# Kernel tuning notes

Hardware: AMD Instinct MI355X
Metric: run time of the kernel (lower is better)

The kernel has to match this reference:

```python
import jax, jax.numpy as jnp
import numpy as np

LN_EPS = 1e-5

def _layernorm(x, g, b):
    m = jnp.mean(x, axis=-1, keepdims=True)
    v = jnp.mean((x - m) ** 2, axis=-1, keepdims=True)
    return (x - m) / jnp.sqrt(v + LN_EPS) * g + b

def _mlp(x, w1, g1, b1, w2, g2, b2):
    # Linear(no bias) -> LayerNorm -> Linear(no bias) -> LayerNorm -> ReLU
    x = _layernorm(x @ w1, g1, b1)
    x = _layernorm(x @ w2, g2, b2)
    return jax.nn.relu(x)

def setup_inputs() -> dict:
    key = jax.random.key(0)
    ks = jax.random.split(key, 16)
    Lc, Lf, N, Dc, Df, K = 1024, 4096, 32, 256, 128, 8
    inv = lambda d: 1.0 / np.sqrt(d)
    inp = {
        "features_coarse": jax.random.normal(ks[0], (Lc, N, Dc), dtype=jnp.float32),
        "features_fine": jax.random.normal(ks[1], (Lf, N, Df), dtype=jnp.float32),
        # mlp_coarse: d_in=Dc, d_ff=Df, d_out=Df
        "w1c": jax.random.uniform(ks[2], (Dc, Df), jnp.float32, -inv(Dc), inv(Dc)),
        "g1c": jnp.ones((Df,), jnp.float32),
        "b1c": jnp.zeros((Df,), jnp.float32),
        "w2c": jax.random.uniform(ks[3], (Df, Df), jnp.float32, -inv(Df), inv(Df)),
        "g2c": jnp.ones((Df,), jnp.float32),
        "b2c": jnp.zeros((Df,), jnp.float32),
        # mlp_fine: d_in=Df, d_ff=Df, d_out=Df
        "w1f": jax.random.uniform(ks[4], (Df, Df), jnp.float32, -inv(Df), inv(Df)),
        "g1f": jnp.ones((Df,), jnp.float32),
        "b1f": jnp.zeros((Df,), jnp.float32),
        "w2f": jax.random.uniform(ks[5], (Df, Df), jnp.float32, -inv(Df), inv(Df)),
        "g2f": jnp.ones((Df,), jnp.float32),
        "b2f": jnp.zeros((Df,), jnp.float32),
        "neighbor_row": jax.random.randint(ks[6], (K * Lc * N,), 0, Lf, dtype=jnp.int64 if jax.config.jax_enable_x64 else jnp.int32),
        "neighbor_col": jax.random.randint(ks[7], (K * Lc * N,), 0, N, dtype=jnp.int64 if jax.config.jax_enable_x64 else jnp.int32),
        "keep_idx": jax.random.randint(ks[8], (Lc,), 0, Lf, dtype=jnp.int64 if jax.config.jax_enable_x64 else jnp.int32),
    }
    return inp

def reference(features_coarse, features_fine, w1c, g1c, b1c, w2c, g2c, b2c,
              w1f, g1f, b1f, w2f, g2f, b2f, neighbor_row, neighbor_col, keep_idx):
    Lc, N, Dc = features_coarse.shape
    Lf, _, Df = features_fine.shape
    D = Df
    fc = _mlp(features_coarse, w1c, g1c, b1c, w2c, g2c, b2c)  # (Lc, N, D)
    ff = _mlp(features_fine, w1f, g1f, b1f, w2f, g2f, b2f)    # (Lf, N, D)
    gathered = ff[neighbor_row, neighbor_col]                  # (K*Lc*N, D)
    updated = fc[None] + gathered.reshape(-1, Lc, N, D)        # (K, Lc, N, D)
    ff = ff.at[neighbor_row, neighbor_col].set(updated.reshape(-1, D))
    return ff
```

## Files before the change

### kernel.cpp

```cpp
#include <hip/hip_runtime.h>
#include <hip/hip_bf16.h>

typedef __attribute__((ext_vector_type(8))) short s8v;
typedef __attribute__((ext_vector_type(4))) float f4v;

__device__ __forceinline__ short f2bf(float f) {
    __hip_bfloat16 h = __float2bfloat16(f);
    union { __hip_bfloat16 h; short s; } u{h};
    return u.s;
}
__device__ __forceinline__ float bf2f(unsigned short v) {
    union { unsigned u; float f; } x; x.u = ((unsigned)v) << 16; return x.f;
}

__global__ void pack_kernel(const float* __restrict__ w1c, const float* __restrict__ w2c,
                            const float* __restrict__ w1f, const float* __restrict__ w2f,
                            short* __restrict__ p1c, short* __restrict__ p2c,
                            short* __restrict__ p1f, short* __restrict__ p2f)
{
    int id = blockIdx.x * 256 + threadIdx.x;
    int f  = id >> 6, l = id & 63;
    const float* W; short* P; int fl;
    if      (f < 64)  { W = w1c; P = p1c; fl = f; }
    else if (f < 96)  { W = w2c; P = p2c; fl = f - 64; }
    else if (f < 128) { W = w1f; P = p1f; fl = f - 96; }
    else              { W = w2f; P = p2f; fl = f - 128; }
    int g = l >> 4, c = l & 15;
    int ks = fl >> 3, n = fl & 7;
    s8v o;
    #pragma unroll
    for (int e = 0; e < 8; ++e)
        o[e] = f2bf(W[(ks*32 + g*8 + e) * 128 + n*16 + c]);
    *(s8v*)(P + ((fl*64 + l) << 3)) = o;
}

template<int K1, bool FINE>
__global__ __launch_bounds__(256, 4)
void mlp_mfma(const float* __restrict__ X,
              const short* __restrict__ Wp1,
              const float* __restrict__ g1v, const float* __restrict__ b1v,
              const short* __restrict__ Wp2,
              const float* __restrict__ g2v, const float* __restrict__ b2v,
              float* __restrict__ outF,
              unsigned short* __restrict__ outB,
              const int* __restrict__ winner,
              const unsigned short* __restrict__ fcB,
              const int* __restrict__ nr, const int* __restrict__ nc,
              int* __restrict__ win, int nWinBlocks)
{
    __shared__ short H[4][16][128];

    if (blockIdx.x < (unsigned)nWinBlocks) {
        int i = blockIdx.x * 256 + threadIdx.x;
        atomicMax(&win[nr[i] * 32 + nc[i]], i);
        return;
    }
    const int bid = blockIdx.x - nWinBlocks;

    const int t = threadIdx.x;
    const int wave = t >> 6, lane = t & 63;
    const int g = lane >> 4, c = lane & 15;
    const int wrow = bid * 64 + wave * 16;

    int wv = 0;
    if constexpr (FINE) wv = winner[wrow + c];

    float G1[8], B1[8];
    #pragma unroll
    for (int n = 0; n < 8; ++n) { G1[n] = g1v[n*16 + c]; B1[n] = b1v[n*16 + c]; }

    f4v acc[8];
    #pragma unroll
    for (int n = 0; n < 8; ++n) acc[n] = (f4v){0.f, 0.f, 0.f, 0.f};

    const float* pa = X + (size_t)(wrow + c) * K1 + g*8;
    const short* wp1 = Wp1 + (lane << 3);
    float4 a0 = *(const float4*)pa;
    float4 a1 = *(const float4*)(pa + 4);
    #pragma unroll
    for (int ks = 0; ks < K1/32; ++ks) {
        s8v bfr[8];
        #pragma unroll
        for (int n = 0; n < 8; ++n)
            bfr[n] = *(const s8v*)(wp1 + ((ks*8 + n) << 9));
        s8v af;
        af[0] = f2bf(a0.x); af[1] = f2bf(a0.y); af[2] = f2bf(a0.z); af[3] = f2bf(a0.w);
        af[4] = f2bf(a1.x); af[5] = f2bf(a1.y); af[6] = f2bf(a1.z); af[7] = f2bf(a1.w);
        if (ks + 1 < K1/32) {
            a0 = *(const float4*)(pa + (ks+1)*32);
            a1 = *(const float4*)(pa + (ks+1)*32 + 4);
        }
        #pragma unroll
        for (int n = 0; n < 8; ++n)
            acc[n] = __builtin_amdgcn_mfma_f32_16x16x32_bf16(af, bfr[n], acc[n], 0, 0, 0);
    }

    #pragma unroll
    for (int j = 0; j < 4; ++j) {
        float sm = 0.f, sq = 0.f;
        #pragma unroll
        for (int n = 0; n < 8; ++n) { float v = acc[n][j]; sm += v; sq += v*v; }
        #pragma unroll
        for (int m = 1; m < 16; m <<= 1) {
            sm += __shfl_xor(sm, m, 64);
            sq += __shfl_xor(sq, m, 64);
        }
        float mean = sm * (1.f/128.f);
        float rstd = rsqrtf(sq * (1.f/128.f) - mean*mean + 1e-5f);
        int row = g*4 + j;
        #pragma unroll
        for (int n = 0; n < 8; ++n) {
            float y = (acc[n][j] - mean) * rstd * G1[n] + B1[n];
            int col = n*16 + c;
            int phys = (((col >> 3) ^ row) << 3) | (col & 7);
            H[wave][row][phys] = f2bf(y);
        }
    }

    f4v acc2[8];
    #pragma unroll
    for (int n = 0; n < 8; ++n) acc2[n] = (f4v){0.f, 0.f, 0.f, 0.f};

    const short* wp2 = Wp2 + (lane << 3);
    #pragma unroll
    for (int ks = 0; ks < 4; ++ks) {
        s8v bfr[8];
        #pragma unroll
        for (int n = 0; n < 8; ++n)
            bfr[n] = *(const s8v*)(wp2 + ((ks*8 + n) << 9));
        s8v af = *(const s8v*)&H[wave][c][((ks*4 + g) ^ c) << 3];
        #pragma unroll
        for (int n = 0; n < 8; ++n)
            acc2[n] = __builtin_amdgcn_mfma_f32_16x16x32_bf16(af, bfr[n], acc2[n], 0, 0, 0);
    }

    float G2[8], B2[8];
    #pragma unroll
    for (int n = 0; n < 8; ++n) { G2[n] = g2v[n*16 + c]; B2[n] = b2v[n*16 + c]; }
    #pragma unroll
    for (int j = 0; j < 4; ++j) {
        float sm = 0.f, sq = 0.f;
        #pragma unroll
        for (int n = 0; n < 8; ++n) { float v = acc2[n][j]; sm += v; sq += v*v; }
        #pragma unroll
        for (int m = 1; m < 16; m <<= 1) {
            sm += __shfl_xor(sm, m, 64);
            sq += __shfl_xor(sq, m, 64);
        }
        float mean = sm * (1.f/128.f);
        float rstd = rsqrtf(sq * (1.f/128.f) - mean*mean + 1e-5f);
        int R = wrow + g*4 + j;
        float y[8];
        #pragma unroll
        for (int n = 0; n < 8; ++n)
            y[n] = fmaxf((acc2[n][j] - mean) * rstd * G2[n] + B2[n], 0.f);
        if constexpr (FINE) {
            int w = __shfl(wv, g*4 + j, 64);
            if (w >= 0) {
                const unsigned short* fp = fcB + (size_t)(w & 32767) * 128 + c;
                #pragma unroll
                for (int n = 0; n < 8; ++n) y[n] += bf2f(fp[n*16]);
            }
            float* op = outF + (size_t)R * 128 + c;
            #pragma unroll
            for (int n = 0; n < 8; ++n) op[n*16] = y[n];
        } else {
            unsigned short* op = outB + (size_t)R * 128 + c;
            #pragma unroll
            for (int n = 0; n < 8; ++n) op[n*16] = (unsigned short)f2bf(y[n]);
        }
    }
}

extern "C" void kernel_launch(void* const* d_in, const int* in_sizes, int n_in,
                              void* d_out, int out_size, void* d_ws, size_t ws_size,
                              hipStream_t stream)
{
    const float* fcoarse = (const float*)d_in[0];
    const float* ffine   = (const float*)d_in[1];
    const float* w1c = (const float*)d_in[2];
    const float* g1c = (const float*)d_in[3];
    const float* b1c = (const float*)d_in[4];
    const float* w2c = (const float*)d_in[5];
    const float* g2c = (const float*)d_in[6];
    const float* b2c = (const float*)d_in[7];
    const float* w1f = (const float*)d_in[8];
    const float* g1f = (const float*)d_in[9];
    const float* b1f = (const float*)d_in[10];
    const float* w2f = (const float*)d_in[11];
    const float* g2f = (const float*)d_in[12];
    const float* b2f = (const float*)d_in[13];
    const int* nrow  = (const int*)d_in[14];
    const int* ncol  = (const int*)d_in[15];

    float* out = (float*)d_out;

    const int Mc = 32768, Mf = 131072;

    unsigned short* fcB = (unsigned short*)d_ws;
    char* base = (char*)d_ws;
    int*   winner = (int*)(base + 8u*1024*1024);
    short* p1c = (short*)(base + 8u*1024*1024 + 512u*1024);
    short* p2c = p1c + 256*128;
    short* p1f = p2c + 128*128;
    short* p2f = p1f + 128*128;

    hipMemsetAsync(winner, 0xFF, (size_t)Mf * sizeof(int), stream);
    pack_kernel<<<40, 256, 0, stream>>>(w1c, w2c, w1f, w2f, p1c, p2c, p1f, p2f);

    mlp_mfma<256, false><<<1024 + Mc/64, 256, 0, stream>>>(
        fcoarse, p1c, g1c, b1c, p2c, g2c, b2c,
        nullptr, fcB, nullptr, nullptr,
        nrow, ncol, winner, 1024);

    mlp_mfma<128, true><<<Mf/64, 256, 0, stream>>>(
        ffine, p1f, g1f, b1f, p2f, g2f, b2f,
        out, nullptr, winner, fcB,
        nullptr, nullptr, nullptr, 0);
}
```

Baseline: 81.04 us.

## Process 64 rows per wave to reuse weight fragments and vectorize output stores

```diff
diff --git a/kernel.cpp b/kernel.cpp
--- a/kernel.cpp
+++ b/kernel.cpp
@@ -35,7 +35,7 @@
 }
 
 template<int K1, bool FINE>
-__global__ __launch_bounds__(256, 4)
+__global__ __launch_bounds__(256, 2)
 void mlp_mfma(const float* __restrict__ X,
               const short* __restrict__ Wp1,
               const float* __restrict__ g1v, const float* __restrict__ b1v,
@@ -48,7 +48,7 @@
               const int* __restrict__ nr, const int* __restrict__ nc,
               int* __restrict__ win, int nWinBlocks)
 {
-    __shared__ short H[4][16][128];
+    __shared__ short H[4][64][128];
 
     if (blockIdx.x < (unsigned)nWinBlocks) {
         int i = blockIdx.x * 256 + threadIdx.x;
@@ -60,66 +60,76 @@
     const int t = threadIdx.x;
     const int wave = t >> 6, lane = t & 63;
     const int g = lane >> 4, c = lane & 15;
-    const int wrow = bid * 64 + wave * 16;
+    const int wrow = bid * 256 + wave * 64;
 
     int wv = 0;
-    if constexpr (FINE) wv = winner[wrow + c];
+    if constexpr (FINE) wv = winner[wrow + lane];
 
     float G1[8], B1[8];
     #pragma unroll
     for (int n = 0; n < 8; ++n) { G1[n] = g1v[n*16 + c]; B1[n] = b1v[n*16 + c]; }
 
-    f4v acc[8];
-    #pragma unroll
-    for (int n = 0; n < 8; ++n) acc[n] = (f4v){0.f, 0.f, 0.f, 0.f};
-
-    const float* pa = X + (size_t)(wrow + c) * K1 + g*8;
+    f4v acc[4][8];
+    #pragma unroll
+    for (int s = 0; s < 4; ++s)
+        #pragma unroll
+        for (int n = 0; n < 8; ++n) acc[s][n] = (f4v){0.f, 0.f, 0.f, 0.f};
+
     const short* wp1 = Wp1 + (lane << 3);
-    float4 a0 = *(const float4*)pa;
-    float4 a1 = *(const float4*)(pa + 4);
     #pragma unroll
     for (int ks = 0; ks < K1/32; ++ks) {
         s8v bfr[8];
         #pragma unroll
         for (int n = 0; n < 8; ++n)
             bfr[n] = *(const s8v*)(wp1 + ((ks*8 + n) << 9));
-        s8v af;
-        af[0] = f2bf(a0.x); af[1] = f2bf(a0.y); af[2] = f2bf(a0.z); af[3] = f2bf(a0.w);
-        af[4] = f2bf(a1.x); af[5] = f2bf(a1.y); af[6] = f2bf(a1.z); af[7] = f2bf(a1.w);
-        if (ks + 1 < K1/32) {
-            a0 = *(const float4*)(pa + (ks+1)*32);
-            a1 = *(const float4*)(pa + (ks+1)*32 + 4);
-        }
-        #pragma unroll
-        for (int n = 0; n < 8; ++n)
-            acc[n] = __builtin_amdgcn_mfma_f32_16x16x32_bf16(af, bfr[n], acc[n], 0, 0, 0);
-    }
-
-    #pragma unroll
-    for (int j = 0; j < 4; ++j) {
-        float sm = 0.f, sq = 0.f;
-        #pragma unroll
-        for (int n = 0; n < 8; ++n) { float v = acc[n][j]; sm += v; sq += v*v; }
-        #pragma unroll
-        for (int m = 1; m < 16; m <<= 1) {
-            sm += __shfl_xor(sm, m, 64);
-            sq += __shfl_xor(sq, m, 64);
-        }
-        float mean = sm * (1.f/128.f);
-        float rstd = rsqrtf(sq * (1.f/128.f) - mean*mean + 1e-5f);
-        int row = g*4 + j;
-        #pragma unroll
-        for (int n = 0; n < 8; ++n) {
-            float y = (acc[n][j] - mean) * rstd * G1[n] + B1[n];
-            int col = n*16 + c;
-            int phys = (((col >> 3) ^ row) << 3) | (col & 7);
-            H[wave][row][phys] = f2bf(y);
-        }
-    }
-
-    f4v acc2[8];
-    #pragma unroll
-    for (int n = 0; n < 8; ++n) acc2[n] = (f4v){0.f, 0.f, 0.f, 0.f};
+        s8v af[4];
+        #pragma unroll
+        for (int s = 0; s < 4; ++s) {
+            const float* p = X + (size_t)(wrow + s*16 + c) * K1 + ks*32 + g*8;
+            float4 a0 = *(const float4*)p;
+            float4 a1 = *(const float4*)(p + 4);
+            s8v v;
+            v[0] = f2bf(a0.x); v[1] = f2bf(a0.y); v[2] = f2bf(a0.z); v[3] = f2bf(a0.w);
+            v[4] = f2bf(a1.x); v[5] = f2bf(a1.y); v[6] = f2bf(a1.z); v[7] = f2bf(a1.w);
+            af[s] = v;
+        }
+        #pragma unroll
+        for (int s = 0; s < 4; ++s)
+            #pragma unroll
+            for (int n = 0; n < 8; ++n)
+                acc[s][n] = __builtin_amdgcn_mfma_f32_16x16x32_bf16(af[s], bfr[n], acc[s][n], 0, 0, 0);
+    }
+
+    #pragma unroll
+    for (int s = 0; s < 4; ++s) {
+        #pragma unroll
+        for (int j = 0; j < 4; ++j) {
+            float sm = 0.f, sq = 0.f;
+            #pragma unroll
+            for (int n = 0; n < 8; ++n) { float v = acc[s][n][j]; sm += v; sq += v*v; }
+            #pragma unroll
+            for (int m = 1; m < 16; m <<= 1) {
+                sm += __shfl_xor(sm, m, 64);
+                sq += __shfl_xor(sq, m, 64);
+            }
+            float mean = sm * (1.f/128.f);
+            float rstd = rsqrtf(sq * (1.f/128.f) - mean*mean + 1e-5f);
+            int row = s*16 + g*4 + j;
+            #pragma unroll
+            for (int n = 0; n < 8; ++n) {
+                float y = (acc[s][n][j] - mean) * rstd * G1[n] + B1[n];
+                int col = n*16 + c;
+                int phys = (((col >> 3) ^ (row & 15)) << 3) | (col & 7);
+                H[wave][row][phys] = f2bf(y);
+            }
+        }
+    }
+
+    f4v acc2[4][8];
+    #pragma unroll
+    for (int s = 0; s < 4; ++s)
+        #pragma unroll
+        for (int n = 0; n < 8; ++n) acc2[s][n] = (f4v){0.f, 0.f, 0.f, 0.f};
 
     const short* wp2 = Wp2 + (lane << 3);
     #pragma unroll
@@ -128,46 +138,67 @@
         #pragma unroll
         for (int n = 0; n < 8; ++n)
             bfr[n] = *(const s8v*)(wp2 + ((ks*8 + n) << 9));
-        s8v af = *(const s8v*)&H[wave][c][((ks*4 + g) ^ c) << 3];
-        #pragma unroll
-        for (int n = 0; n < 8; ++n)
-            acc2[n] = __builtin_amdgcn_mfma_f32_16x16x32_bf16(af, bfr[n], acc2[n], 0, 0, 0);
+        s8v af[4];
+        #pragma unroll
+        for (int s = 0; s < 4; ++s)
+            af[s] = *(const s8v*)&H[wave][s*16 + c][((ks*4 + g) ^ c) << 3];
+        #pragma unroll
+        for (int s = 0; s < 4; ++s)
+            #pragma unroll
+            for (int n = 0; n < 8; ++n)
+                acc2[s][n] = __builtin_amdgcn_mfma_f32_16x16x32_bf16(af[s], bfr[n], acc2[s][n], 0, 0, 0);
     }
 
     float G2[8], B2[8];
     #pragma unroll
     for (int n = 0; n < 8; ++n) { G2[n] = g2v[n*16 + c]; B2[n] = b2v[n*16 + c]; }
     #pragma unroll
-    for (int j = 0; j < 4; ++j) {
-        float sm = 0.f, sq = 0.f;
-        #pragma unroll
-        for (int n = 0; n < 8; ++n) { float v = acc2[n][j]; sm += v; sq += v*v; }
-        #pragma unroll
-        for (int m = 1; m < 16; m <<= 1) {
-            sm += __shfl_xor(sm, m, 64);
-            sq += __shfl_xor(sq, m, 64);
-        }
-        float mean = sm * (1.f/128.f);
-        float rstd = rsqrtf(sq * (1.f/128.f) - mean*mean + 1e-5f);
-        int R = wrow + g*4 + j;
-        float y[8];
-        #pragma unroll
-        for (int n = 0; n < 8; ++n)
-            y[n] = fmaxf((acc2[n][j] - mean) * rstd * G2[n] + B2[n], 0.f);
+    for (int s = 0; s < 4; ++s) {
+        #pragma unroll
+        for (int j = 0; j < 4; ++j) {
+            float sm = 0.f, sq = 0.f;
+            #pragma unroll
+            for (int n = 0; n < 8; ++n) { float v = acc2[s][n][j]; sm += v; sq += v*v; }
+            #pragma unroll
+            for (int m = 1; m < 16; m <<= 1) {
+                sm += __shfl_xor(sm, m, 64);
+                sq += __shfl_xor(sq, m, 64);
+            }
+            float mean = sm * (1.f/128.f);
+            float rstd = rsqrtf(sq * (1.f/128.f) - mean*mean + 1e-5f);
+            int row = s*16 + g*4 + j;
+            #pragma unroll
+            for (int n = 0; n < 8; ++n) {
+                float y = fmaxf((acc2[s][n][j] - mean) * rstd * G2[n] + B2[n], 0.f);
+                int col = n*16 + c;
+                int phys = (((col >> 3) ^ (row & 15)) << 3) | (col & 7);
+                H[wave][row][phys] = f2bf(y);
+            }
+        }
+    }
+
+    #pragma unroll
+    for (int it = 0; it < 16; ++it) {
+        int row = it*4 + g;
+        int R   = wrow + row;
+        s8v v = *(const s8v*)&H[wave][row][(c ^ (row & 15)) << 3];
         if constexpr (FINE) {
-            int w = __shfl(wv, g*4 + j, 64);
+            float y8[8];
+            #pragma unroll
+            for (int e = 0; e < 8; ++e) y8[e] = bf2f((unsigned short)v[e]);
+            int w = __shfl(wv, row, 64);
             if (w >= 0) {
-                const unsigned short* fp = fcB + (size_t)(w & 32767) * 128 + c;
+                const s8v u = *(const s8v*)(fcB + (size_t)(w & 32767) * 128 + c*8);
                 #pragma unroll
-                for (int n = 0; n < 8; ++n) y[n] += bf2f(fp[n*16]);
-            }
-            float* op = outF + (size_t)R * 128 + c;
-            #pragma unroll
-            for (int n = 0; n < 8; ++n) op[n*16] = y[n];
+                for (int e = 0; e < 8; ++e) y8[e] += bf2f((unsigned short)u[e]);
+            }
+            float4 o0 = {y8[0], y8[1], y8[2], y8[3]};
+            float4 o1 = {y8[4], y8[5], y8[6], y8[7]};
+            float* op = outF + (size_t)R * 128 + c*8;
+            *(float4*)op       = o0;
+            *(float4*)(op + 4) = o1;
         } else {
-            unsigned short* op = outB + (size_t)R * 128 + c;
-            #pragma unroll
-            for (int n = 0; n < 8; ++n) op[n*16] = (unsigned short)f2bf(y[n]);
+            *(s8v*)(outB + (size_t)R * 128 + c*8) = v;
         }
     }
 }
@@ -208,12 +239,12 @@
     hipMemsetAsync(winner, 0xFF, (size_t)Mf * sizeof(int), stream);
     pack_kernel<<<40, 256, 0, stream>>>(w1c, w2c, w1f, w2f, p1c, p2c, p1f, p2f);
 
-    mlp_mfma<256, false><<<1024 + Mc/64, 256, 0, stream>>>(
+    mlp_mfma<256, false><<<1024 + Mc/256, 256, 0, stream>>>(
         fcoarse, p1c, g1c, b1c, p2c, g2c, b2c,
         nullptr, fcB, nullptr, nullptr,
         nrow, ncol, winner, 1024);
 
-    mlp_mfma<128, true><<<Mf/64, 256, 0, stream>>>(
+    mlp_mfma<128, true><<<Mf/256, 256, 0, stream>>>(
         ffine, p1f, g1f, b1f, p2f, g2f, b2f,
         out, nullptr, winner, fcB,
         nullptr, nullptr, nullptr, 0);
```

New measurement: 121.9 us. +50.5%, slower.

## Fold first LayerNorm into second GEMM weights and pass activations via shuffles

Applied to the files above, without the earlier changes.

```diff
diff --git a/kernel.cpp b/kernel.cpp
--- a/kernel.cpp
+++ b/kernel.cpp
@@ -12,34 +12,62 @@
 __device__ __forceinline__ float bf2f(unsigned short v) {
     union { unsigned u; float f; } x; x.u = ((unsigned)v) << 16; return x.f;
 }
-
-__global__ void pack_kernel(const float* __restrict__ w1c, const float* __restrict__ w2c,
+__device__ __forceinline__ unsigned packbf(float a, float b) {
+    return (unsigned)(unsigned short)f2bf(a) | ((unsigned)(unsigned short)f2bf(b) << 16);
+}
+
+__global__ void prep_kernel(const float* __restrict__ w1c, const float* __restrict__ w2c,
+                            const float* __restrict__ g1c, const float* __restrict__ b1c,
                             const float* __restrict__ w1f, const float* __restrict__ w2f,
+                            const float* __restrict__ g1f, const float* __restrict__ b1f,
                             short* __restrict__ p1c, short* __restrict__ p2c,
-                            short* __restrict__ p1f, short* __restrict__ p2f)
+                            short* __restrict__ p1f, short* __restrict__ p2f,
+                            float* __restrict__ s2c, float* __restrict__ bwc,
+                            float* __restrict__ s2f, float* __restrict__ bwf)
 {
-    int id = blockIdx.x * 256 + threadIdx.x;
+    int b = blockIdx.x, t = threadIdx.x;
+    if (b >= 40) {
+        if (t >= 128) return;
+        const float* W  = (b == 40) ? w2c : w2f;
+        const float* g1 = (b == 40) ? g1c : g1f;
+        const float* b1 = (b == 40) ? b1c : b1f;
+        float* s2 = (b == 40) ? s2c : s2f;
+        float* bw = (b == 40) ? bwc : bwf;
+        float s = 0.f, w2sum = 0.f;
+        for (int k = 0; k < 128; ++k) {
+            float wv = W[k * 128 + t];
+            s     += bf2f((unsigned short)f2bf(g1[k] * wv));
+            w2sum += b1[k] * wv;
+        }
+        s2[t] = s; bw[t] = w2sum;
+        return;
+    }
+    int id = b * 256 + t;
     int f  = id >> 6, l = id & 63;
-    const float* W; short* P; int fl;
+    const float* W; const float* g1 = nullptr; short* P; int fl;
     if      (f < 64)  { W = w1c; P = p1c; fl = f; }
-    else if (f < 96)  { W = w2c; P = p2c; fl = f - 64; }
+    else if (f < 96)  { W = w2c; P = p2c; fl = f - 64;  g1 = g1c; }
     else if (f < 128) { W = w1f; P = p1f; fl = f - 96; }
-    else              { W = w2f; P = p2f; fl = f - 128; }
+    else              { W = w2f; P = p2f; fl = f - 128; g1 = g1f; }
     int g = l >> 4, c = l & 15;
     int ks = fl >> 3, n = fl & 7;
     s8v o;
     #pragma unroll
-    for (int e = 0; e < 8; ++e)
-        o[e] = f2bf(W[(ks*32 + g*8 + e) * 128 + n*16 + c]);
+    for (int e = 0; e < 8; ++e) {
+        int k = ks*32 + g*8 + e;
+        float v = W[k * 128 + n*16 + c];
+        if (g1) v *= g1[k];
+        o[e] = f2bf(v);
+    }
     *(s8v*)(P + ((fl*64 + l) << 3)) = o;
 }
 
 template<int K1, bool FINE>
 __global__ __launch_bounds__(256, 4)
 void mlp_mfma(const float* __restrict__ X,
-              const short* __restrict__ Wp1,
-              const float* __restrict__ g1v, const float* __restrict__ b1v,
-              const short* __restrict__ Wp2,
+              const short* __restrict__ WpA,
+              const short* __restrict__ WpB,
+              const float* __restrict__ s2v, const float* __restrict__ bwv,
               const float* __restrict__ g2v, const float* __restrict__ b2v,
               float* __restrict__ outF,
               unsigned short* __restrict__ outB,
@@ -48,126 +76,156 @@
               const int* __restrict__ nr, const int* __restrict__ nc,
               int* __restrict__ win, int nWinBlocks)
 {
-    __shared__ short H[4][16][128];
-
     if (blockIdx.x < (unsigned)nWinBlocks) {
         int i = blockIdx.x * 256 + threadIdx.x;
         atomicMax(&win[nr[i] * 32 + nc[i]], i);
         return;
     }
-    const int bid = blockIdx.x - nWinBlocks;
-
-    const int t = threadIdx.x;
+    const int bid  = blockIdx.x - nWinBlocks;
+    const int t    = threadIdx.x;
     const int wave = t >> 6, lane = t & 63;
-    const int g = lane >> 4, c = lane & 15;
-    const int wrow = bid * 64 + wave * 16;
+    const int G = lane >> 4, n16 = lane & 15;
+    const int row = bid * 64 + wave * 16 + n16;
+    const size_t rowK = (size_t)row * K1;
 
     int wv = 0;
-    if constexpr (FINE) wv = winner[wrow + c];
-
-    float G1[8], B1[8];
-    #pragma unroll
-    for (int n = 0; n < 8; ++n) { G1[n] = g1v[n*16 + c]; B1[n] = b1v[n*16 + c]; }
-
-    f4v acc[8];
-    #pragma unroll
-    for (int n = 0; n < 8; ++n) acc[n] = (f4v){0.f, 0.f, 0.f, 0.f};
-
-    const float* pa = X + (size_t)(wrow + c) * K1 + g*8;
-    const short* wp1 = Wp1 + (lane << 3);
-    float4 a0 = *(const float4*)pa;
-    float4 a1 = *(const float4*)(pa + 4);
-    #pragma unroll
-    for (int ks = 0; ks < K1/32; ++ks) {
-        s8v bfr[8];
-        #pragma unroll
-        for (int n = 0; n < 8; ++n)
-            bfr[n] = *(const s8v*)(wp1 + ((ks*8 + n) << 9));
-        s8v af;
-        af[0] = f2bf(a0.x); af[1] = f2bf(a0.y); af[2] = f2bf(a0.z); af[3] = f2bf(a0.w);
-        af[4] = f2bf(a1.x); af[5] = f2bf(a1.y); af[6] = f2bf(a1.z); af[7] = f2bf(a1.w);
-        if (ks + 1 < K1/32) {
-            a0 = *(const float4*)(pa + (ks+1)*32);
-            a1 = *(const float4*)(pa + (ks+1)*32 + 4);
-        }
-        #pragma unroll
-        for (int n = 0; n < 8; ++n)
-            acc[n] = __builtin_amdgcn_mfma_f32_16x16x32_bf16(af, bfr[n], acc[n], 0, 0, 0);
-    }
-
-    #pragma unroll
-    for (int j = 0; j < 4; ++j) {
-        float sm = 0.f, sq = 0.f;
-        #pragma unroll
-        for (int n = 0; n < 8; ++n) { float v = acc[n][j]; sm += v; sq += v*v; }
-        #pragma unroll
-        for (int m = 1; m < 16; m <<= 1) {
-            sm += __shfl_xor(sm, m, 64);
-            sq += __shfl_xor(sq, m, 64);
-        }
-        float mean = sm * (1.f/128.f);
-        float rstd = rsqrtf(sq * (1.f/128.f) - mean*mean + 1e-5f);
-        int row = g*4 + j;
-        #pragma unroll
-        for (int n = 0; n < 8; ++n) {
-            float y = (acc[n][j] - mean) * rstd * G1[n] + B1[n];
-            int col = n*16 + c;
-            int phys = (((col >> 3) ^ row) << 3) | (col & 7);
-            H[wave][row][phys] = f2bf(y);
-        }
+    if constexpr (FINE) wv = winner[row];
+
+    f4v acc1[8];
+    #pragma unroll
+    for (int mt = 0; mt < 8; ++mt) acc1[mt] = (f4v){0.f, 0.f, 0.f, 0.f};
+
+    const short* wpa = WpA + (lane << 3);
+    const float* pX  = X + rowK + G*8;
+    #pragma unroll
+    for (int kb = 0; kb < K1/32; kb += 4) {
+        float4 aPf[4][2];
+        #pragma unroll
+        for (int k2 = 0; k2 < 4; ++k2) {
+            aPf[k2][0] = *(const float4*)(pX + (kb + k2)*32);
+            aPf[k2][1] = *(const float4*)(pX + (kb + k2)*32 + 4);
+        }
+        #pragma unroll
+        for (int k2 = 0; k2 < 4; ++k2) {
+            const int ks = kb + k2;
+            s8v wfr[8];
+            #pragma unroll
+            for (int mt = 0; mt < 8; ++mt)
+                wfr[mt] = *(const s8v*)(wpa + ((ks*8 + mt) << 9));
+            s8v xf;
+            xf[0] = f2bf(aPf[k2][0].x); xf[1] = f2bf(aPf[k2][0].y);
+            xf[2] = f2bf(aPf[k2][0].z); xf[3] = f2bf(aPf[k2][0].w);
+            xf[4] = f2bf(aPf[k2][1].x); xf[5] = f2bf(aPf[k2][1].y);
+            xf[6] = f2bf(aPf[k2][1].z); xf[7] = f2bf(aPf[k2][1].w);
+            #pragma unroll
+            for (int mt = 0; mt < 8; ++mt)
+                acc1[mt] = __builtin_amdgcn_mfma_f32_16x16x32_bf16(wfr[mt], xf, acc1[mt], 0, 0, 0);
+        }
+    }
+
+    float sm = 0.f, sq = 0.f;
+    #pragma unroll
+    for (int mt = 0; mt < 8; ++mt)
+        #pragma unroll
+        for (int j = 0; j < 4; ++j) { float v = acc1[mt][j]; sm += v; sq += v*v; }
+    sm += __shfl_xor(sm, 16, 64); sm += __shfl_xor(sm, 32, 64);
+    sq += __shfl_xor(sq, 16, 64); sq += __shfl_xor(sq, 32, 64);
+    const float mean1 = sm * (1.f/128.f);
+    const float rstd1 = rsqrtf(sq * (1.f/128.f) - mean1*mean1 + 1e-5f);
+
+    unsigned pk[8][2];
+    #pragma unroll
+    for (int mt = 0; mt < 8; ++mt) {
+        pk[mt][0] = packbf(acc1[mt][0], acc1[mt][1]);
+        pk[mt][1] = packbf(acc1[mt][2], acc1[mt][3]);
     }
 
     f4v acc2[8];
     #pragma unroll
-    for (int n = 0; n < 8; ++n) acc2[n] = (f4v){0.f, 0.f, 0.f, 0.f};
-
-    const short* wp2 = Wp2 + (lane << 3);
+    for (int mt = 0; mt < 8; ++mt) acc2[mt] = (f4v){0.f, 0.f, 0.f, 0.f};
+
+    const short* wpb = WpB + (lane << 3);
+    const int src0 = ((G & 1) << 5) + n16;
+    const int src1 = src0 + 16;
+    const bool hiG = (G >= 2);
     #pragma unroll
     for (int ks = 0; ks < 4; ++ks) {
-        s8v bfr[8];
-        #pragma unroll
-        for (int n = 0; n < 8; ++n)
-            bfr[n] = *(const s8v*)(wp2 + ((ks*8 + n) << 9));
-        s8v af = *(const s8v*)&H[wave][c][((ks*4 + g) ^ c) << 3];
-        #pragma unroll
-        for (int n = 0; n < 8; ++n)
-            acc2[n] = __builtin_amdgcn_mfma_f32_16x16x32_bf16(af, bfr[n], acc2[n], 0, 0, 0);
-    }
-
-    float G2[8], B2[8];
-    #pragma unroll
-    for (int n = 0; n < 8; ++n) { G2[n] = g2v[n*16 + c]; B2[n] = b2v[n*16 + c]; }
-    #pragma unroll
-    for (int j = 0; j < 4; ++j) {
-        float sm = 0.f, sq = 0.f;
-        #pragma unroll
-        for (int n = 0; n < 8; ++n) { float v = acc2[n][j]; sm += v; sq += v*v; }
-        #pragma unroll
-        for (int m = 1; m < 16; m <<= 1) {
-            sm += __shfl_xor(sm, m, 64);
-            sq += __shfl_xor(sq, m, 64);
-        }
-        float mean = sm * (1.f/128.f);
-        float rstd = rsqrtf(sq * (1.f/128.f) - mean*mean + 1e-5f);
-        int R = wrow + g*4 + j;
-        float y[8];
-        #pragma unroll
-        for (int n = 0; n < 8; ++n)
-            y[n] = fmaxf((acc2[n][j] - mean) * rstd * G2[n] + B2[n], 0.f);
-        if constexpr (FINE) {
-            int w = __shfl(wv, g*4 + j, 64);
-            if (w >= 0) {
-                const unsigned short* fp = fcB + (size_t)(w & 32767) * 128 + c;
-                #pragma unroll
-                for (int n = 0; n < 8; ++n) y[n] += bf2f(fp[n*16]);
+        int r00 = __shfl((int)pk[2*ks][0],   src0, 64);
+        int r01 = __shfl((int)pk[2*ks][1],   src0, 64);
+        int r02 = __shfl((int)pk[2*ks][0],   src1, 64);
+        int r03 = __shfl((int)pk[2*ks][1],   src1, 64);
+        int r10 = __shfl((int)pk[2*ks+1][0], src0, 64);
+        int r11 = __shfl((int)pk[2*ks+1][1], src0, 64);
+        int r12 = __shfl((int)pk[2*ks+1][0], src1, 64);
+        int r13 = __shfl((int)pk[2*ks+1][1], src1, 64);
+        union { int u[4]; s8v v; } hb;
+        hb.u[0] = hiG ? r10 : r00; hb.u[1] = hiG ? r11 : r01;
+        hb.u[2] = hiG ? r12 : r02; hb.u[3] = hiG ? r13 : r03;
+        s8v wfr[8];
+        #pragma unroll
+        for (int mt = 0; mt < 8; ++mt)
+            wfr[mt] = *(const s8v*)(wpb + ((ks*8 + mt) << 9));
+        #pragma unroll
+        for (int mt = 0; mt < 8; ++mt)
+            acc2[mt] = __builtin_amdgcn_mfma_f32_16x16x32_bf16(wfr[mt], hb.v, acc2[mt], 0, 0, 0);
+    }
+
+    float h2[8][4];
+    float sm2 = 0.f, sq2 = 0.f;
+    #pragma unroll
+    for (int mt = 0; mt < 8; ++mt) {
+        const int col = mt*16 + G*4;
+        f4v s2l = *(const f4v*)&s2v[col];
+        f4v bwl = *(const f4v*)&bwv[col];
+        #pragma unroll
+        for (int j = 0; j < 4; ++j) {
+            float v = rstd1 * (acc2[mt][j] - mean1 * s2l[j]) + bwl[j];
+            h2[mt][j] = v; sm2 += v; sq2 += v*v;
+        }
+    }
+    sm2 += __shfl_xor(sm2, 16, 64); sm2 += __shfl_xor(sm2, 32, 64);
+    sq2 += __shfl_xor(sq2, 16, 64); sq2 += __shfl_xor(sq2, 32, 64);
+    const float mean2 = sm2 * (1.f/128.f);
+    const float rstd2 = rsqrtf(sq2 * (1.f/128.f) - mean2*mean2 + 1e-5f);
+
+    if constexpr (FINE) {
+        ushort4 gv[8];
+        const bool hasw = (wv >= 0);
+        const size_t src = (size_t)(wv & 32767) * 128;
+        if (hasw) {
+            #pragma unroll
+            for (int mt = 0; mt < 8; ++mt)
+                gv[mt] = *(const ushort4*)(fcB + src + mt*16 + G*4);
+        }
+        #pragma unroll
+        for (int mt = 0; mt < 8; ++mt) {
+            const int col = mt*16 + G*4;
+            f4v g2l = *(const f4v*)&g2v[col];
+            f4v b2l = *(const f4v*)&b2v[col];
+            float4 o;
+            float z0 = fmaxf((h2[mt][0]-mean2)*rstd2*g2l[0] + b2l[0], 0.f);
+            float z1 = fmaxf((h2[mt][1]-mean2)*rstd2*g2l[1] + b2l[1], 0.f);
+            float z2 = fmaxf((h2[mt][2]-mean2)*rstd2*g2l[2] + b2l[2], 0.f);
+            float z3 = fmaxf((h2[mt][3]-mean2)*rstd2*g2l[3] + b2l[3], 0.f);
+            if (hasw) {
+                z0 += bf2f(gv[mt].x); z1 += bf2f(gv[mt].y);
+                z2 += bf2f(gv[mt].z); z3 += bf2f(gv[mt].w);
             }
-            float* op = outF + (size_t)R * 128 + c;
-            #pragma unroll
-            for (int n = 0; n < 8; ++n) op[n*16] = y[n];
-        } else {
-            unsigned short* op = outB + (size_t)R * 128 + c;
-            #pragma unroll
-            for (int n = 0; n < 8; ++n) op[n*16] = (unsigned short)f2bf(y[n]);
+            o.x = z0; o.y = z1; o.z = z2; o.w = z3;
+            *(float4*)(outF + (size_t)row * 128 + col) = o;
+        }
+    } else {
+        #pragma unroll
+        for (int mt = 0; mt < 8; ++mt) {
+            const int col = mt*16 + G*4;
+            f4v g2l = *(const f4v*)&g2v[col];
+            f4v b2l = *(const f4v*)&b2v[col];
+            ushort4 o;
+            o.x = (unsigned short)f2bf(fmaxf((h2[mt][0]-mean2)*rstd2*g2l[0] + b2l[0], 0.f));
+            o.y = (unsigned short)f2bf(fmaxf((h2[mt][1]-mean2)*rstd2*g2l[1] + b2l[1], 0.f));
+            o.z = (unsigned short)f2bf(fmaxf((h2[mt][2]-mean2)*rstd2*g2l[2] + b2l[2], 0.f));
+            o.w = (unsigned short)f2bf(fmaxf((h2[mt][3]-mean2)*rstd2*g2l[3] + b2l[3], 0.f));
+            *(ushort4*)(outB + (size_t)row * 128 + col) = o;
         }
     }
 }
@@ -194,7 +252,6 @@
     const int* ncol  = (const int*)d_in[15];
 
     float* out = (float*)d_out;
-
     const int Mc = 32768, Mf = 131072;
 
     unsigned short* fcB = (unsigned short*)d_ws;
@@ -204,17 +261,22 @@
     short* p2c = p1c + 256*128;
     short* p1f = p2c + 128*128;
     short* p2f = p1f + 128*128;
+    float* s2c = (float*)(p2f + 128*128);
+    float* bwc = s2c + 128;
+    float* s2f = bwc + 128;
+    float* bwf = s2f + 128;
 
     hipMemsetAsync(winner, 0xFF, (size_t)Mf * sizeof(int), stream);
-    pack_kernel<<<40, 256, 0, stream>>>(w1c, w2c, w1f, w2f, p1c, p2c, p1f, p2f);
+    prep_kernel<<<42, 256, 0, stream>>>(w1c, w2c, g1c, b1c, w1f, w2f, g1f, b1f,
+                                        p1c, p2c, p1f, p2f, s2c, bwc, s2f, bwf);
 
     mlp_mfma<256, false><<<1024 + Mc/64, 256, 0, stream>>>(
-        fcoarse, p1c, g1c, b1c, p2c, g2c, b2c,
+        fcoarse, p1c, p2c, s2c, bwc, g2c, b2c,
         nullptr, fcB, nullptr, nullptr,
         nrow, ncol, winner, 1024);
 
     mlp_mfma<128, true><<<Mf/64, 256, 0, stream>>>(
-        ffine, p1f, g1f, b1f, p2f, g2f, b2f,
+        ffine, p1f, p2f, s2f, bwf, g2f, b2f,
         out, nullptr, winner, fcB,
         nullptr, nullptr, nullptr, 0);
 }
```

After: 93.16 us. 1.15x slower.
